# Kernel optimization log

Measured on AMD Instinct MI355X. Metric: run time of the kernel, lower is better.

Reference implementation:

```python
import jax, jax.numpy as jnp
import numpy as np

N = 8192
IN_F = 256
OUT_F = 64
ALPHA = 0.2  # LeakyReLU negative slope
NEG_INF = -9e15


def setup_inputs() -> dict:
    key = jax.random.key(0)
    k1, k2, k3, k4 = jax.random.split(key, 4)
    input_h = jax.random.normal(k1, (N, IN_F), dtype=jnp.float32)
    # xavier_normal with gain=1.414 ~ std = 1.414*sqrt(2/(fan_in+fan_out))
    W = jax.random.normal(k2, (IN_F, OUT_F), dtype=jnp.float32) * (1.414 * np.sqrt(2.0 / (IN_F + OUT_F)))
    a = jax.random.normal(k3, (2 * OUT_F, 1), dtype=jnp.float32) * (1.414 * np.sqrt(2.0 / (2 * OUT_F + 1)))
    adj = jax.random.randint(k4, (N, N), 0, 2).astype(jnp.int32)
    return {"input_h": input_h, "adj": adj, "W": W, "a": a}


def reference(input_h, adj, W, a):
    # h = X @ W : [N, OUT_F]
    h = input_h @ W
    # Pairwise concat score: a^T [h_i || h_j] == (h_i @ a1) + (h_j @ a2)
    a1 = a[:OUT_F]   # [OUT_F, 1]
    a2 = a[OUT_F:]   # [OUT_F, 1]
    f1 = h @ a1      # [N, 1] -> contribution of source node i
    f2 = h @ a2      # [N, 1] -> contribution of target node j
    e = jax.nn.leaky_relu(f1 + f2.T, negative_slope=ALPHA)  # [N, N]
    # Masked softmax over neighbors (adj > 0), dropout is identity in eval mode
    attention = jax.nn.softmax(jnp.where(adj > 0, e, NEG_INF), axis=-1)
    h_prime = attention @ h  # [N, OUT_F]
    # concat=True -> ELU activation
    return jax.nn.elu(h_prime)
```

## Files before the change

### kernel.cpp

```cpp
#include <hip/hip_runtime.h>
#include <hip/hip_bf16.h>


using short8 = __attribute__((ext_vector_type(8))) short;
using f32x4  = __attribute__((ext_vector_type(4))) float;

#define NN     8192
#define INF_   256
#define OUTF   64
#define LR_A   0.2f
#define LOG2E  1.4426950408889634f
#define ROWS   16
#define TILE_C 128
#define CQW    2048
#define NTILES (CQW / TILE_C)
#define ADJSLOT 8192
#define HPSLOT  16384

__device__ __forceinline__ unsigned short f2bf_rne(float x) {
  unsigned int u = __float_as_uint(x);
  u += 0x7FFFu + ((u >> 16) & 1u);
  return (unsigned short)(u >> 16);
}

__global__ __launch_bounds__(256) void gat_pre(
    const float* __restrict__ input, const float* __restrict__ W,
    const float* __restrict__ a, unsigned short* __restrict__ hp,
    float* __restrict__ f1, float* __restrict__ f2) {
  __shared__ float WT[OUTF][260];
  int tid = threadIdx.x;
  for (int idx = tid; idx < INF_ * OUTF; idx += 256) {
    int c = idx >> 6, f = idx & 63;
    WT[f][c] = W[idx];
  }
  __syncthreads();
  int w = tid >> 6, l = tid & 63;
  int i0 = blockIdx.x * 16 + w * 4;
  const float4* r0 = (const float4*)(input + (long)(i0 + 0) * INF_);
  const float4* r1 = (const float4*)(input + (long)(i0 + 1) * INF_);
  const float4* r2 = (const float4*)(input + (long)(i0 + 2) * INF_);
  const float4* r3 = (const float4*)(input + (long)(i0 + 3) * INF_);
  float h0 = 0.f, h1 = 0.f, h2 = 0.f, h3 = 0.f;
#pragma unroll 4
  for (int c4 = 0; c4 < INF_ / 4; ++c4) {
    float4 wv = *(const float4*)&WT[l][c4 * 4];
    float4 v0 = r0[c4], v1 = r1[c4], v2 = r2[c4], v3 = r3[c4];
    h0 = fmaf(v0.x, wv.x, h0); h0 = fmaf(v0.y, wv.y, h0);
    h0 = fmaf(v0.z, wv.z, h0); h0 = fmaf(v0.w, wv.w, h0);
    h1 = fmaf(v1.x, wv.x, h1); h1 = fmaf(v1.y, wv.y, h1);
    h1 = fmaf(v1.z, wv.z, h1); h1 = fmaf(v1.w, wv.w, h1);
    h2 = fmaf(v2.x, wv.x, h2); h2 = fmaf(v2.y, wv.y, h2);
    h2 = fmaf(v2.z, wv.z, h2); h2 = fmaf(v2.w, wv.w, h2);
    h3 = fmaf(v3.x, wv.x, h3); h3 = fmaf(v3.y, wv.y, h3);
    h3 = fmaf(v3.z, wv.z, h3); h3 = fmaf(v3.w, wv.w, h3);
  }
  float a1k = a[l], a2k = a[OUTF + l];
  float hh[4] = {h0, h1, h2, h3};
#pragma unroll
  for (int r = 0; r < 4; ++r) {
    int i = i0 + r;
    float t1 = hh[r] * a1k, t2 = hh[r] * a2k;
#pragma unroll
    for (int off = 32; off; off >>= 1) {
      t1 += __shfl_xor(t1, off);
      t2 += __shfl_xor(t2, off);
    }
    int gran = (((i >> 5) * 4) + (l >> 4)) * 64 + ((i >> 3) & 3) * 16 + (l & 15);
    hp[(long)gran * 8 + (i & 7)] = f2bf_rne(hh[r]);
    if (l == 0) { f1[i] = t1 * LOG2E; f2[i] = t2 * LOG2E; }
  }
}

__global__ __launch_bounds__(256, 2) void gat_main(
    const int* __restrict__ adj, const unsigned short* __restrict__ hp,
    const float* __restrict__ f1, const float* __restrict__ f2,
    float* __restrict__ numP, float* __restrict__ denP) {
  __shared__ __align__(16) char adjS[3 * ADJSLOT];
  __shared__ __align__(16) char hpS[2 * HPSLOT];
  __shared__ float f2s[CQW];
  __shared__ float ssum[4][ROWS];
  __shared__ float f1s[ROWS], shifts[ROWS], red[4];
  int tid = threadIdx.x;
  int w = tid >> 6, l = tid & 63;
  int i0 = blockIdx.x * ROWS;
  int cq = blockIdx.y;

  float fm = -1e30f;
  for (int jj = tid * 4; jj < NN; jj += 1024) {
    float4 v = *(const float4*)(f2 + jj);
    fm = fmaxf(fm, fmaxf(fmaxf(v.x, v.y), fmaxf(v.z, v.w)));
  }
  for (int jj = tid * 4; jj < CQW; jj += 1024)
    *(float4*)&f2s[jj] = *(const float4*)(f2 + cq * CQW + jj);
#pragma unroll
  for (int off = 32; off; off >>= 1) fm = fmaxf(fm, __shfl_xor(fm, off));
  if (l == 0) red[w] = fm;
  __syncthreads();
  if (tid == 0) red[0] = fmaxf(fmaxf(red[0], red[1]), fmaxf(red[2], red[3]));
  __syncthreads();
  float Fmax = red[0];
  if (tid < ROWS) {
    float v = f1[i0 + tid];
    f1s[tid] = v;
    float s = v + Fmax;
    shifts[tid] = fmaxf(s, LR_A * s);
  }
  __syncthreads();

  int q = l & 15, g = l >> 4;
  float f1r = f1s[q], sh = shifts[q];
  float u1 = f1r - sh, u2 = LR_A * f1r - sh;
  f32x4 acc0 = {0.f, 0.f, 0.f, 0.f}, acc1 = acc0, acc2 = acc0, acc3 = acc0;
  float srow = 0.f;

  auto stage_adj = [&](int t, int slot) {
#pragma unroll
    for (int j = 0; j < 2; ++j) {
      int rr = w * 4 + j * 2 + (l >> 5);
      const int* src = adj + (long)(i0 + rr) * NN + cq * CQW + t * TILE_C
                       + (((l & 31) ^ (rr & 7)) << 2);
      char* d = adjS + slot * ADJSLOT + (w * 4 + j * 2) * 512;
      __builtin_amdgcn_global_load_lds(
          (const __attribute__((address_space(1))) void*)src,
          (__attribute__((address_space(3))) void*)d, 16, 0, 0);
    }
  };
  auto stage_hp = [&](int t, int slot) {
    const unsigned short* base = hp + (long)(cq * 64 + t * 4 + w) * 2048 + l * 8;
#pragma unroll
    for (int j = 0; j < 4; ++j) {
      const unsigned short* src = base + j * 512;
      char* d = hpS + slot * HPSLOT + w * 4096 + j * 1024;
      __builtin_amdgcn_global_load_lds(
          (const __attribute__((address_space(1))) void*)src,
          (__attribute__((address_space(3))) void*)d, 16, 0, 0);
    }
  };

  stage_hp(0, 0);
  stage_adj(0, 0);
  stage_adj(1, 1);

  for (int t = 0; t < NTILES; ++t) {
    if (t < NTILES - 1) {
      asm volatile("s_waitcnt vmcnt(2)" ::: "memory");
    } else {
      asm volatile("s_waitcnt vmcnt(0)" ::: "memory");
    }
    __builtin_amdgcn_s_barrier();
    if (t + 1 < NTILES) stage_hp(t + 1, (t + 1) & 1);
    if (t + 2 < NTILES) stage_adj(t + 2, (t + 2) % 3);

    const char* ab = adjS + (t % 3) * ADJSLOT + q * 512;
    int koff = w * 128 + g * 32;
    int sw = (q & 7) << 4;
    int4 A0 = *(const int4*)(ab + (koff ^ sw));
    int4 A1 = *(const int4*)(ab + ((koff + 16) ^ sw));
    const float* f2b = f2s + t * TILE_C + w * 32 + g * 8;
    float4 F0 = *(const float4*)(f2b);
    float4 F1 = *(const float4*)(f2b + 4);
    float fa[8] = {F0.x, F0.y, F0.z, F0.w, F1.x, F1.y, F1.z, F1.w};
    int   aa[8] = {A0.x, A0.y, A0.z, A0.w, A1.x, A1.y, A1.z, A1.w};

    union { short8 v; unsigned short u[8]; } pa;
    float ps = 0.f;
#pragma unroll
    for (int e = 0; e < 8; ++e) {
      float arg = fmaxf(u1 + fa[e], fmaf(LR_A, fa[e], u2));
      float pe = (aa[e] > 0) ? exp2f(arg) : 0.f;
      ps += pe;
      pa.u[e] = f2bf_rne(pe);
    }
    srow += ps;

    const unsigned short* hb =
        (const unsigned short*)(hpS + (t & 1) * HPSLOT + w * 4096) + l * 8;
    short8 b0 = *(const short8*)(hb + 0 * 512);
    short8 b1 = *(const short8*)(hb + 1 * 512);
    short8 b2 = *(const short8*)(hb + 2 * 512);
    short8 b3 = *(const short8*)(hb + 3 * 512);
    acc0 = __builtin_amdgcn_mfma_f32_16x16x32_bf16(pa.v, b0, acc0, 0, 0, 0);
    acc1 = __builtin_amdgcn_mfma_f32_16x16x32_bf16(pa.v, b1, acc1, 0, 0, 0);
    acc2 = __builtin_amdgcn_mfma_f32_16x16x32_bf16(pa.v, b2, acc2, 0, 0, 0);
    acc3 = __builtin_amdgcn_mfma_f32_16x16x32_bf16(pa.v, b3, acc3, 0, 0, 0);
  }

  srow += __shfl_xor(srow, 16);
  srow += __shfl_xor(srow, 32);

  __syncthreads();
  if (l < ROWS) ssum[w][l] = srow;
  float* accs = (float*)hpS;
#pragma unroll
  for (int r = 0; r < 4; ++r) {
    accs[(w * ROWS + g * 4 + r) * OUTF + 0 * 16 + q] = acc0[r];
    accs[(w * ROWS + g * 4 + r) * OUTF + 1 * 16 + q] = acc1[r];
    accs[(w * ROWS + g * 4 + r) * OUTF + 2 * 16 + q] = acc2[r];
    accs[(w * ROWS + g * 4 + r) * OUTF + 3 * 16 + q] = acc3[r];
  }
  __syncthreads();

  for (int idx = tid; idx < ROWS * OUTF; idx += 256) {
    int m = idx >> 6, n = idx & 63;
    float num = 0.f, den = 0.f;
#pragma unroll
    for (int ww = 0; ww < 4; ++ww) {
      num += accs[(ww * ROWS + m) * OUTF + n];
      den += ssum[ww][m];
    }
    numP[((long)cq * NN + i0 + m) * OUTF + n] = num;
    if (n == 0) denP[(long)cq * NN + i0 + m] = den;
  }
}

__global__ __launch_bounds__(256) void gat_fin(
    const float* __restrict__ numP, const float* __restrict__ denP,
    float* __restrict__ out) {
  int gid = blockIdx.x * 256 + threadIdx.x;
  int row = gid >> 6, n = gid & 63;
  float num = 0.f, den = 0.f;
#pragma unroll
  for (int c = 0; c < 4; ++c) {
    num += numP[((long)c * NN + row) * OUTF + n];
    den += denP[(long)c * NN + row];
  }
  float v = num / den;
  out[gid] = v > 0.f ? v : expm1f(v);
}

extern "C" void kernel_launch(void* const* d_in, const int* in_sizes, int n_in,
                              void* d_out, int out_size, void* d_ws, size_t ws_size,
                              hipStream_t stream) {
  const float* input = (const float*)d_in[0];
  const int*   adj   = (const int*)d_in[1];
  const float* W     = (const float*)d_in[2];
  const float* a     = (const float*)d_in[3];
  float* out = (float*)d_out;
  char* ws = (char*)d_ws;
  unsigned short* hp = (unsigned short*)ws;
  float* f1   = (float*)(ws + (1 << 20));
  float* f2   = (float*)(ws + (1 << 20) + (32 << 10));
  float* numP = (float*)(ws + (1 << 20) + (64 << 10));
  float* denP = (float*)(ws + (1 << 20) + (64 << 10) + (8 << 20));
  (void)in_sizes; (void)n_in; (void)out_size; (void)ws_size;

  gat_pre<<<512, 256, 0, stream>>>(input, W, a, hp, f1, f2);
  gat_main<<<dim3(512, 4), 256, 0, stream>>>(adj, hp, f1, f2, numP, denP);
  gat_fin<<<NN * OUTF / 256, 256, 0, stream>>>(numP, denP, out);
}
```

Baseline: 121.8 us.

## Load hp operands directly to registers and register-stage adj to cut LDS

Replaces the async global-to-LDS staging of adjacency and bf16 h tiles with a register-prefetch pipeline. h fragments are loaded straight into registers one tile ahead and fed to MFMA without going through LDS. Adjacency tiles are loaded into registers two tiles ahead, then written into a double-buffered swizzled LDS slot. This cuts LDS use from about 57KB to about 24KB and raises the occupancy target to 3 blocks per CU. The trade-off is more registers, two barriers per tile, and synchronous loads that may leave global latency less hidden.

```diff
diff --git a/kernel.cpp b/kernel.cpp
--- a/kernel.cpp
+++ b/kernel.cpp
@@ -5,17 +5,16 @@
 using short8 = __attribute__((ext_vector_type(8))) short;
 using f32x4  = __attribute__((ext_vector_type(4))) float;
 
-#define NN     8192
-#define INF_   256
-#define OUTF   64
-#define LR_A   0.2f
-#define LOG2E  1.4426950408889634f
-#define ROWS   16
-#define TILE_C 128
-#define CQW    2048
-#define NTILES (CQW / TILE_C)
+#define NN      8192
+#define INF_    256
+#define OUTF    64
+#define LR_A    0.2f
+#define LOG2E   1.4426950408889634f
+#define ROWS    16
+#define TILE_C  128
+#define CQW     2048
+#define NTILES  (CQW / TILE_C)
 #define ADJSLOT 8192
-#define HPSLOT  16384
 
 __device__ __forceinline__ unsigned short f2bf_rne(float x) {
   unsigned int u = __float_as_uint(x);
@@ -71,12 +70,11 @@
   }
 }
 
-__global__ __launch_bounds__(256, 2) void gat_main(
+__global__ __launch_bounds__(256, 3) void gat_main(
     const int* __restrict__ adj, const unsigned short* __restrict__ hp,
     const float* __restrict__ f1, const float* __restrict__ f2,
     float* __restrict__ numP, float* __restrict__ denP) {
-  __shared__ __align__(16) char adjS[3 * ADJSLOT];
-  __shared__ __align__(16) char hpS[2 * HPSLOT];
+  __shared__ __align__(16) char adjS[2 * ADJSLOT];
   __shared__ float f2s[CQW];
   __shared__ float ssum[4][ROWS];
   __shared__ float f1s[ROWS], shifts[ROWS], red[4];
@@ -113,55 +111,44 @@
   f32x4 acc0 = {0.f, 0.f, 0.f, 0.f}, acc1 = acc0, acc2 = acc0, acc3 = acc0;
   float srow = 0.f;
 
-  auto stage_adj = [&](int t, int slot) {
-#pragma unroll
-    for (int j = 0; j < 2; ++j) {
-      int rr = w * 4 + j * 2 + (l >> 5);
-      const int* src = adj + (long)(i0 + rr) * NN + cq * CQW + t * TILE_C
-                       + (((l & 31) ^ (rr & 7)) << 2);
-      char* d = adjS + slot * ADJSLOT + (w * 4 + j * 2) * 512;
-      __builtin_amdgcn_global_load_lds(
-          (const __attribute__((address_space(1))) void*)src,
-          (__attribute__((address_space(3))) void*)d, 16, 0, 0);
-    }
-  };
-  auto stage_hp = [&](int t, int slot) {
+  int l5 = l >> 5, l31 = l & 31;
+  int r0_ = w * 4 + l5;
+  int r1_ = r0_ + 2;
+  const int* adjb = adj + cq * CQW + (long)i0 * NN;
+  int xw0 = (l31 * 16) ^ ((r0_ & 7) << 4);
+  int xw1 = (l31 * 16) ^ ((r1_ & 7) << 4);
+  int xo = (q & 7) << 4;
+
+  int4 aA[2], aB[2];
+  short8 hA[4], hB[4];
+
+  auto load_adj = [&](int4* d, int t) {
+    const int* c0 = adjb + (long)r0_ * NN + t * TILE_C + l31 * 4;
+    const int* c1 = adjb + (long)r1_ * NN + t * TILE_C + l31 * 4;
+    d[0] = *(const int4*)c0;
+    d[1] = *(const int4*)c1;
+  };
+  auto load_hp = [&](short8* d, int t) {
     const unsigned short* base = hp + (long)(cq * 64 + t * 4 + w) * 2048 + l * 8;
 #pragma unroll
-    for (int j = 0; j < 4; ++j) {
-      const unsigned short* src = base + j * 512;
-      char* d = hpS + slot * HPSLOT + w * 4096 + j * 1024;
-      __builtin_amdgcn_global_load_lds(
-          (const __attribute__((address_space(1))) void*)src,
-          (__attribute__((address_space(3))) void*)d, 16, 0, 0);
-    }
-  };
-
-  stage_hp(0, 0);
-  stage_adj(0, 0);
-  stage_adj(1, 1);
-
-  for (int t = 0; t < NTILES; ++t) {
-    if (t < NTILES - 1) {
-      asm volatile("s_waitcnt vmcnt(2)" ::: "memory");
-    } else {
-      asm volatile("s_waitcnt vmcnt(0)" ::: "memory");
-    }
-    __builtin_amdgcn_s_barrier();
-    if (t + 1 < NTILES) stage_hp(t + 1, (t + 1) & 1);
-    if (t + 2 < NTILES) stage_adj(t + 2, (t + 2) % 3);
-
-    const char* ab = adjS + (t % 3) * ADJSLOT + q * 512;
+    for (int nb = 0; nb < 4; ++nb) d[nb] = *(const short8*)(base + nb * 512);
+  };
+  auto store_adj = [&](int s, const int4* d) {
+    char* b = adjS + s * ADJSLOT;
+    *(int4*)(b + r0_ * 512 + xw0) = d[0];
+    *(int4*)(b + r1_ * 512 + xw1) = d[1];
+  };
+
+  auto compute = [&](int t, const short8* hC) {
+    const char* ab = adjS + (t & 1) * ADJSLOT + q * 512;
     int koff = w * 128 + g * 32;
-    int sw = (q & 7) << 4;
-    int4 A0 = *(const int4*)(ab + (koff ^ sw));
-    int4 A1 = *(const int4*)(ab + ((koff + 16) ^ sw));
+    int4 A0 = *(const int4*)(ab + (koff ^ xo));
+    int4 A1 = *(const int4*)(ab + ((koff + 16) ^ xo));
     const float* f2b = f2s + t * TILE_C + w * 32 + g * 8;
     float4 F0 = *(const float4*)(f2b);
     float4 F1 = *(const float4*)(f2b + 4);
     float fa[8] = {F0.x, F0.y, F0.z, F0.w, F1.x, F1.y, F1.z, F1.w};
     int   aa[8] = {A0.x, A0.y, A0.z, A0.w, A1.x, A1.y, A1.z, A1.w};
-
     union { short8 v; unsigned short u[8]; } pa;
     float ps = 0.f;
 #pragma unroll
@@ -172,17 +159,35 @@
       pa.u[e] = f2bf_rne(pe);
     }
     srow += ps;
-
-    const unsigned short* hb =
-        (const unsigned short*)(hpS + (t & 1) * HPSLOT + w * 4096) + l * 8;
-    short8 b0 = *(const short8*)(hb + 0 * 512);
-    short8 b1 = *(const short8*)(hb + 1 * 512);
-    short8 b2 = *(const short8*)(hb + 2 * 512);
-    short8 b3 = *(const short8*)(hb + 3 * 512);
-    acc0 = __builtin_amdgcn_mfma_f32_16x16x32_bf16(pa.v, b0, acc0, 0, 0, 0);
-    acc1 = __builtin_amdgcn_mfma_f32_16x16x32_bf16(pa.v, b1, acc1, 0, 0, 0);
-    acc2 = __builtin_amdgcn_mfma_f32_16x16x32_bf16(pa.v, b2, acc2, 0, 0, 0);
-    acc3 = __builtin_amdgcn_mfma_f32_16x16x32_bf16(pa.v, b3, acc3, 0, 0, 0);
+    acc0 = __builtin_amdgcn_mfma_f32_16x16x32_bf16(pa.v, hC[0], acc0, 0, 0, 0);
+    acc1 = __builtin_amdgcn_mfma_f32_16x16x32_bf16(pa.v, hC[1], acc1, 0, 0, 0);
+    acc2 = __builtin_amdgcn_mfma_f32_16x16x32_bf16(pa.v, hC[2], acc2, 0, 0, 0);
+    acc3 = __builtin_amdgcn_mfma_f32_16x16x32_bf16(pa.v, hC[3], acc3, 0, 0, 0);
+  };
+
+  auto body = [&](int t, int4* aPn, int4* aPnn, short8* hC, short8* hN) {
+    __builtin_amdgcn_sched_barrier(0);
+    __builtin_amdgcn_s_barrier();
+    if (t + 1 < NTILES) store_adj((t + 1) & 1, aPn);
+    if (t + 2 < NTILES) load_adj(aPnn, t + 2);
+    if (t + 1 < NTILES) load_hp(hN, t + 1);
+    asm volatile("s_waitcnt lgkmcnt(0)" ::: "memory");
+    __builtin_amdgcn_sched_barrier(0);
+    __builtin_amdgcn_s_barrier();
+    compute(t, hC);
+  };
+
+  load_adj(aA, 0);
+  store_adj(0, aA);
+  load_adj(aA, 1);
+  load_hp(hA, 0);
+  asm volatile("s_waitcnt lgkmcnt(0)" ::: "memory");
+  __builtin_amdgcn_sched_barrier(0);
+  __builtin_amdgcn_s_barrier();
+
+  for (int tt = 0; tt < NTILES; tt += 2) {
+    body(tt, aA, aB, hA, hB);
+    body(tt + 1, aB, aA, hB, hA);
   }
 
   srow += __shfl_xor(srow, 16);
@@ -190,7 +195,7 @@
 
   __syncthreads();
   if (l < ROWS) ssum[w][l] = srow;
-  float* accs = (float*)hpS;
+  float* accs = (float*)adjS;
 #pragma unroll
   for (int r = 0; r < 4; ++r) {
     accs[(w * ROWS + g * 4 + r) * OUTF + 0 * 16 + q] = acc0[r];
```

New measurement: 159.1 us. 30.7% more time.
